# Kernel tuning notes

Measured on AMD Instinct MI355X. Metric: run time of the kernel, lower is better.

## Reference

```python
import jax, jax.numpy as jnp
import numpy as np

B, N, D = 8, 2048, 3
HIDDEN = (64, 128, 256)
LATENT = 128


def _layernorm(x, scale, bias, eps=1e-6):
    mu = jnp.mean(x, axis=-1, keepdims=True)
    var = jnp.mean((x - mu) ** 2, axis=-1, keepdims=True)
    return (x - mu) / jnp.sqrt(var + eps) * scale + bias


def setup_inputs() -> dict:
    key = jax.random.key(0)
    ks = jax.random.split(key, 8)
    inp = {
        "x": jax.random.normal(ks[0], (B, N, D), dtype=jnp.float32),
        "mask": jnp.ones((B, N), dtype=jnp.float32),
    }
    in_d = D
    for i, d in enumerate(HIDDEN):
        inp[f"W{i}"] = (jax.random.normal(ks[1 + i], (in_d, d), dtype=jnp.float32)
                        / np.float32(np.sqrt(in_d)))
        inp[f"b{i}"] = jnp.zeros((d,), dtype=jnp.float32)
        inp[f"g{i}"] = jnp.ones((d,), dtype=jnp.float32)
        inp[f"be{i}"] = jnp.zeros((d,), dtype=jnp.float32)
        in_d = d
    inp["Wz"] = (jax.random.normal(ks[5], (in_d, LATENT), dtype=jnp.float32)
                 / np.float32(np.sqrt(in_d)))
    inp["bz"] = jnp.zeros((LATENT,), dtype=jnp.float32)
    return inp


def reference(x, mask, W0, b0, g0, be0, W1, b1, g1, be1, W2, b2, g2, be2, Wz, bz):
    m = mask[..., None]                                   # (B, N, 1)
    count = jnp.sum(m, axis=1)                            # (B, 1)
    centroid = jnp.sum(x * m, axis=1, keepdims=True) / jnp.maximum(count, 1.0)[:, None, :]
    xc = x - centroid                                     # (B, N, D)

    # Pairwise squared distances; attention depends only on coordinates,
    # so it is identical for every layer -> compute once.
    diff = xc[:, :, None, :] - xc[:, None, :, :]          # (B, N, N, D)
    dist = jnp.sum(diff * diff, axis=-1)                  # (B, N, N)
    attn = jax.nn.softmax(-dist, axis=-1)                 # (B, N, N)

    h = xc
    for W, b, g, be in ((W0, b0, g0, be0), (W1, b1, g1, be1), (W2, b2, g2, be2)):
        h_agg = jnp.einsum('bij,bjd->bid', attn, h)       # weighted aggregation
        h = h_agg @ W + b
        h = _layernorm(h, g, be)
        h = jax.nn.swish(h)

    # Invariant readout: masked mean pool then Dense(latent)
    global_feat = jnp.sum(h * m, axis=1) / jnp.maximum(count, 1.0)
    z = global_feat @ Wz + bz                             # (B, latent)
    return z
```

## Files before the change

### kernel.cpp

```cpp
#include <hip/hip_runtime.h>
#include <hip/hip_bf16.h>

#define BATCH 8
#define NPTS 2048
#define LATENT 128

typedef __attribute__((ext_vector_type(8))) short short8;
typedef __attribute__((ext_vector_type(4))) float f32x4;

__device__ __forceinline__ ushort f2bf(float f) {
  unsigned int b = __float_as_uint(f);
  b += 0x7FFF + ((b >> 16) & 1);
  return (ushort)(b >> 16);
}
__device__ __forceinline__ float bf2f(ushort u) {
  return __uint_as_float(((unsigned int)u) << 16);
}
__device__ __forceinline__ unsigned int pkbf(float a, float b) {
  __hip_bfloat162 h = __float22bfloat162_rn(make_float2(a, b));
  return *(unsigned int*)&h;
}

#define L2E 1.4426950408889634f
#define SC2 1.6986436f

__device__ __forceinline__ void wtrans_tile(const float* __restrict__ W,
    ushort* __restrict__ WT, int K, int N, int n0, int k0, int tid) {
  __shared__ ushort s[64][72];
  for (int i = tid; i < 64 * 64; i += 256) {
    const int kl = i >> 6, nl = i & 63;
    s[kl][nl] = f2bf(W[(size_t)(k0 + kl) * N + n0 + nl]);
  }
  __syncthreads();
  for (int i = tid; i < 64 * 64; i += 256) {
    const int nl = i >> 6, kl = i & 63;
    WT[(size_t)(n0 + nl) * K + k0 + kl] = s[kl][nl];
  }
}

__global__ __launch_bounds__(256) void setup_kernel(const float* __restrict__ x,
    const float* __restrict__ mask, float4* __restrict__ pnt,
    const float* __restrict__ W1, ushort* __restrict__ WT1,
    const float* __restrict__ W2, ushort* __restrict__ WT2,
    const float* __restrict__ Wz, ushort* __restrict__ WzT) {
  const int bid = blockIdx.x;
  const int tid = threadIdx.x;
  if (bid >= 8) {
    if (bid < 10) wtrans_tile(W1, WT1, 64, 128, (bid - 8) * 64, 0, tid);
    else if (bid < 18) {
      const int idx = bid - 10;
      wtrans_tile(W2, WT2, 128, 256, (idx & 3) * 64, (idx >> 2) * 64, tid);
    } else {
      const int idx = bid - 18;
      wtrans_tile(Wz, WzT, 256, 128, (idx & 1) * 64, (idx >> 1) * 64, tid);
    }
    return;
  }
  const int b = bid;
  const float* xb = x + (size_t)b * NPTS * 3;
  const float* mb = mask + (size_t)b * NPTS;
  float s0 = 0.f, s1 = 0.f, s2 = 0.f, c = 0.f;
  for (int n = tid; n < NPTS; n += 256) {
    float m = mb[n];
    s0 += xb[n * 3 + 0] * m;
    s1 += xb[n * 3 + 1] * m;
    s2 += xb[n * 3 + 2] * m;
    c += m;
  }
  __shared__ float red[4][256];
  red[0][tid] = s0; red[1][tid] = s1; red[2][tid] = s2; red[3][tid] = c;
  __syncthreads();
  for (int off = 128; off > 0; off >>= 1) {
    if (tid < off) {
      red[0][tid] += red[0][tid + off];
      red[1][tid] += red[1][tid + off];
      red[2][tid] += red[2][tid + off];
      red[3][tid] += red[3][tid + off];
    }
    __syncthreads();
  }
  const float cnt = fmaxf(red[3][0], 1.0f);
  const float c0 = red[0][0] / cnt, c1 = red[1][0] / cnt, c2 = red[2][0] / cnt;
  float4* pb = pnt + (size_t)b * NPTS;
  for (int n = tid; n < NPTS; n += 256) {
    const float a0 = xb[n * 3 + 0] - c0;
    const float a1 = xb[n * 3 + 1] - c1;
    const float a2 = xb[n * 3 + 2] - c2;
    pb[n] = make_float4(a0 * SC2, a1 * SC2, a2 * SC2,
                        -(a0 * a0 + a1 * a1 + a2 * a2) * L2E);
  }
}

__global__ __launch_bounds__(512) void layer0_kernel(
    const float4* __restrict__ pnt, const float* __restrict__ W,
    const float* __restrict__ bias, const float* __restrict__ g,
    const float* __restrict__ be, ushort* __restrict__ hout) {
  const int b = blockIdx.y;
  const int i0 = blockIdx.x * 64;
  const int tid = threadIdx.x;
  const int il = tid & 63, part = tid >> 6;
  const float4* pb = pnt + (size_t)b * NPTS;
  const float4 pi = pb[i0 + il];
  float a0 = 0.f, a1 = 0.f, a2 = 0.f, dn = 0.f;
#pragma unroll 8
  for (int j = part * 256; j < part * 256 + 256; j++) {
    const float4 pj = pb[j];
    float arg = pi.w + pj.w;
    arg = fmaf(pi.x, pj.x, arg);
    arg = fmaf(pi.y, pj.y, arg);
    arg = fmaf(pi.z, pj.z, arg);
    const float w = __builtin_amdgcn_exp2f(arg);
    a0 = fmaf(w, pj.x, a0);
    a1 = fmaf(w, pj.y, a1);
    a2 = fmaf(w, pj.z, a2);
    dn += w;
  }
  __shared__ float4 sred[8][64];
  __shared__ float srow[64 * 3];
  __shared__ ushort lt[64][64];
  sred[part][il] = make_float4(a0, a1, a2, dn);
  __syncthreads();
  if (tid < 64) {
    float A0 = 0.f, A1 = 0.f, A2 = 0.f, DN = 0.f;
#pragma unroll
    for (int p = 0; p < 8; p++) {
      const float4 r = sred[p][tid];
      A0 += r.x; A1 += r.y; A2 += r.z; DN += r.w;
    }
    const float inv = 1.0f / (DN * SC2);
    srow[tid * 3 + 0] = A0 * inv;
    srow[tid * 3 + 1] = A1 * inv;
    srow[tid * 3 + 2] = A2 * inv;
  }
  __syncthreads();
  const int wv = tid >> 6, lane = tid & 63;
  const float w0c = W[lane], w1c = W[64 + lane], w2c = W[128 + lane];
  const float gv = g[lane], bev = be[lane], bv = bias[lane];
#pragma unroll
  for (int r = 0; r < 8; r++) {
    const int row = wv * 8 + r;
    float o = bv;
    o = fmaf(srow[row * 3 + 0], w0c, o);
    o = fmaf(srow[row * 3 + 1], w1c, o);
    o = fmaf(srow[row * 3 + 2], w2c, o);
    float m1 = o, m2 = o * o;
#pragma unroll
    for (int off = 32; off > 0; off >>= 1) {
      m1 += __shfl_xor(m1, off, 64);
      m2 += __shfl_xor(m2, off, 64);
    }
    const float mu = m1 / 64.f;
    const float rstd = rsqrtf(m2 / 64.f - mu * mu + 1e-6f);
    const float v = (o - mu) * rstd * gv + bev;
    const float act = v / (1.0f + __expf(-v));
    lt[row][lane] = f2bf(act);
  }
  __syncthreads();
  if (tid < 64) {
    ushort tmp[64];
#pragma unroll
    for (int r = 0; r < 64; r++) tmp[r] = lt[r][tid];
    ushort* dst = hout + ((size_t)b * 64 + tid) * NPTS + i0;
#pragma unroll
    for (int c = 0; c < 8; c++)
      *(uint4*)(dst + c * 8) = *(uint4*)&tmp[c * 8];
  }
}

template <int DIN, int DOUT, bool POOL, int MINW>
__global__ __launch_bounds__(256, MINW) void fused_layer(
    const float4* __restrict__ pnt, const ushort* __restrict__ hT,
    const ushort* __restrict__ WT, const float* __restrict__ bias,
    const float* __restrict__ g, const float* __restrict__ be,
    ushort* __restrict__ hout, const float* __restrict__ mask,
    float* __restrict__ partial) {
  constexpr int NT = DIN / 16;
  constexpr int QJ = NPTS / 4;
  constexpr int KS = QJ / 32;
  constexpr int NCOL = DOUT / 32;
  constexpr int PS = DIN + 8;
  constexpr int PN = DIN + 4;
  constexpr int SPNT_B = NPTS * 16;
  constexpr int SNUM_B = 32 * PN * 4;
  constexpr int OFF_SROW = SNUM_B;
  constexpr int OFF_SDEN = OFF_SROW + 32 * PS * 2;
  constexpr int OFF_SINV = OFF_SDEN + 128;
  constexpr int OFF_SSTAT = OFF_SINV + 128;
  constexpr int EPI_B = OFF_SSTAT + 512;
  constexpr int SMEM_B = SPNT_B > EPI_B ? SPNT_B : EPI_B;
  __shared__ __align__(16) char smem[SMEM_B];
  float4* sp = (float4*)smem;

  const int b = blockIdx.y;
  const int i0 = blockIdx.x * 32;
  const int tid = threadIdx.x;
  const int wv = tid >> 6, lane = tid & 63;
  const int m = lane & 15, q = lane >> 4;
  const float4* pb = pnt + (size_t)b * NPTS;
  const ushort* hb = hT + (size_t)b * DIN * NPTS;

#pragma unroll
  for (int i = 0; i < NPTS / 256; i++) {
    const int j = i * 256 + tid;
    const int phys = (j & ~31) | (((j & 7) << 2) | ((j >> 3) & 3));
    sp[phys] = pb[j];
  }
  const float4 pi0 = pb[i0 + m];
  const float4 pi1 = pb[i0 + 16 + m];
  __syncthreads();

  f32x4 acc0[NT], acc1[NT];
#pragma unroll
  for (int nt = 0; nt < NT; nt++)
#pragma unroll
    for (int e = 0; e < 4; e++) { acc0[nt][e] = 0.f; acc1[nt][e] = 0.f; }
  float dacc0 = 0.f, dacc1 = 0.f;

  const int jq = wv * QJ;

  for (int k = 0; k < KS; k++) {
    const int j0 = jq + k * 32;
    short8 bq[NT];
#pragma unroll
    for (int nt = 0; nt < NT; nt++)
      bq[nt] = *(const short8*)(hb + (size_t)(nt * 16 + m) * NPTS + j0 + q * 8);
    float w0a[8], w1a[8];
#pragma unroll
    for (int jj = 0; jj < 8; jj++) {
      const float4 pj = sp[j0 + ((jj << 2) | q)];
      float a0 = pi0.w + pj.w;
      a0 = fmaf(pi0.x, pj.x, a0);
      a0 = fmaf(pi0.y, pj.y, a0);
      a0 = fmaf(pi0.z, pj.z, a0);
      float a1 = pi1.w + pj.w;
      a1 = fmaf(pi1.x, pj.x, a1);
      a1 = fmaf(pi1.y, pj.y, a1);
      a1 = fmaf(pi1.z, pj.z, a1);
      w0a[jj] = __builtin_amdgcn_exp2f(a0);
      w1a[jj] = __builtin_amdgcn_exp2f(a1);
      dacc0 += w0a[jj]; dacc1 += w1a[jj];
    }
    unsigned int au0[4], au1[4];
#pragma unroll
    for (int p = 0; p < 4; p++) {
      au0[p] = pkbf(w0a[2 * p], w0a[2 * p + 1]);
      au1[p] = pkbf(w1a[2 * p], w1a[2 * p + 1]);
    }
    const short8 af0 = *(short8*)au0;
    const short8 af1 = *(short8*)au1;
#pragma unroll
    for (int nt = 0; nt < NT; nt++) {
      acc0[nt] = __builtin_amdgcn_mfma_f32_16x16x32_bf16(af0, bq[nt], acc0[nt], 0, 0, 0);
      acc1[nt] = __builtin_amdgcn_mfma_f32_16x16x32_bf16(af1, bq[nt], acc1[nt], 0, 0, 0);
    }
  }
  __syncthreads();

  float* snum = (float*)smem;
  ushort* srow = (ushort*)(smem + OFF_SROW);
  float* sden = (float*)(smem + OFF_SDEN);
  float* sinv = (float*)(smem + OFF_SINV);
  float* sstat = (float*)(smem + OFF_SSTAT);

  dacc0 += __shfl_xor(dacc0, 16, 64);
  dacc0 += __shfl_xor(dacc0, 32, 64);
  dacc1 += __shfl_xor(dacc1, 16, 64);
  dacc1 += __shfl_xor(dacc1, 32, 64);
  for (int p = 0; p < 4; p++) {
    if (wv == p) {
      if (p == 0) {
#pragma unroll
        for (int nt = 0; nt < NT; nt++)
#pragma unroll
          for (int r = 0; r < 4; r++) {
            snum[(q * 4 + r) * PN + nt * 16 + m] = acc0[nt][r];
            snum[(16 + q * 4 + r) * PN + nt * 16 + m] = acc1[nt][r];
          }
        if (q == 0) { sden[m] = dacc0; sden[16 + m] = dacc1; }
      } else {
#pragma unroll
        for (int nt = 0; nt < NT; nt++)
#pragma unroll
          for (int r = 0; r < 4; r++) {
            snum[(q * 4 + r) * PN + nt * 16 + m] += acc0[nt][r];
            snum[(16 + q * 4 + r) * PN + nt * 16 + m] += acc1[nt][r];
          }
        if (q == 0) { sden[m] += dacc0; sden[16 + m] += dacc1; }
      }
    }
    __syncthreads();
  }
  if (tid < 32) sinv[tid] = 1.0f / sden[tid];
  __syncthreads();
  for (int idx = tid; idx < 32 * (DIN / 2); idx += 256) {
    const int r = idx / (DIN / 2), c2 = idx % (DIN / 2);
    const float v0 = snum[r * PN + 2 * c2] * sinv[r];
    const float v1 = snum[r * PN + 2 * c2 + 1] * sinv[r];
    *(unsigned int*)&srow[r * PS + 2 * c2] = pkbf(v0, v1);
  }
  __syncthreads();

  const int rg2 = wv >> 1, ch = wv & 1;
  short8 afrag[DIN / 32];
#pragma unroll
  for (int kt = 0; kt < DIN / 32; kt++)
    afrag[kt] = *(const short8*)&srow[(rg2 * 16 + m) * PS + kt * 32 + q * 8];
  f32x4 oacc[NCOL];
#pragma unroll
  for (int c = 0; c < NCOL; c++)
#pragma unroll
    for (int e = 0; e < 4; e++) oacc[c][e] = 0.f;
#pragma unroll
  for (int c = 0; c < NCOL; c++) {
    const int n0 = (ch * NCOL + c) * 16;
#pragma unroll
    for (int kt = 0; kt < DIN / 32; kt++) {
      const short8 bfrag = *(const short8*)(WT + (size_t)(n0 + m) * DIN + kt * 32 + q * 8);
      oacc[c] = __builtin_amdgcn_mfma_f32_16x16x32_bf16(afrag[kt], bfrag, oacc[c], 0, 0, 0);
    }
  }

  float bcol[NCOL];
#pragma unroll
  for (int c = 0; c < NCOL; c++) bcol[c] = bias[(ch * NCOL + c) * 16 + m];
#pragma unroll
  for (int r = 0; r < 4; r++) {
    float m1 = 0.f, m2 = 0.f;
#pragma unroll
    for (int c = 0; c < NCOL; c++) {
      const float v = oacc[c][r] + bcol[c];
      m1 += v; m2 += v * v;
    }
#pragma unroll
    for (int off = 8; off > 0; off >>= 1) {
      m1 += __shfl_xor(m1, off, 64);
      m2 += __shfl_xor(m2, off, 64);
    }
    if (m == 0) {
      const int row = rg2 * 16 + q * 4 + r;
      sstat[(row * 2 + ch) * 2 + 0] = m1;
      sstat[(row * 2 + ch) * 2 + 1] = m2;
    }
  }
  __syncthreads();

  ushort* lt = (ushort*)smem;
  float* spl = (float*)smem;
  float pacc[NCOL];
  if (POOL) {
#pragma unroll
    for (int c = 0; c < NCOL; c++) pacc[c] = 0.f;
  }
#pragma unroll
  for (int r = 0; r < 4; r++) {
    const int row = rg2 * 16 + q * 4 + r;
    const float m1 = sstat[(row * 2 + 0) * 2 + 0] + sstat[(row * 2 + 1) * 2 + 0];
    const float m2 = sstat[(row * 2 + 0) * 2 + 1] + sstat[(row * 2 + 1) * 2 + 1];
    const float mu = m1 / DOUT;
    const float rstd = rsqrtf(m2 / DOUT - mu * mu + 1e-6f);
    float mval = 0.f;
    if (POOL) mval = mask[(size_t)b * NPTS + i0 + row];
#pragma unroll
    for (int c = 0; c < NCOL; c++) {
      const int dco = (ch * NCOL + c) * 16 + m;
      const float v = (oacc[c][r] + bcol[c] - mu) * rstd * g[dco] + be[dco];
      const float act = v / (1.0f + __expf(-v));
      if (POOL) pacc[c] = fmaf(act, mval, pacc[c]);
      else lt[row * DOUT + dco] = f2bf(act);
    }
  }
  if (POOL) {
#pragma unroll
    for (int c = 0; c < NCOL; c++) {
      float v = pacc[c];
      v += __shfl_xor(v, 16, 64);
      v += __shfl_xor(v, 32, 64);
      if (q == 0) spl[rg2 * DOUT + (ch * NCOL + c) * 16 + m] = v;
    }
    __syncthreads();
    if (tid < DOUT)
      partial[((size_t)b * (NPTS / 32) + blockIdx.x) * DOUT + tid] =
          spl[tid] + spl[DOUT + tid];
  } else {
    __syncthreads();
    if (tid < DOUT) {
      ushort tmp[32];
#pragma unroll
      for (int r = 0; r < 32; r++) tmp[r] = lt[r * DOUT + tid];
      ushort* dst = hout + ((size_t)b * DOUT + tid) * NPTS + i0;
#pragma unroll
      for (int c = 0; c < 4; c++)
        *(uint4*)(dst + c * 8) = *(uint4*)&tmp[c * 8];
    }
  }
}

__global__ __launch_bounds__(256) void readout_kernel(
    const float* __restrict__ partial, const float* __restrict__ mask,
    const ushort* __restrict__ WzT, const float* __restrict__ bz,
    float* __restrict__ out) {
  const int b = blockIdx.x;
  const int tid = threadIdx.x;
  const float* pb = partial + (size_t)b * (NPTS / 32) * 256;
  float s0 = 0.f, s1 = 0.f, s2 = 0.f, s3 = 0.f;
#pragma unroll 4
  for (int p = 0; p < NPTS / 32; p += 4) {
    s0 += pb[(size_t)(p + 0) * 256 + tid];
    s1 += pb[(size_t)(p + 1) * 256 + tid];
    s2 += pb[(size_t)(p + 2) * 256 + tid];
    s3 += pb[(size_t)(p + 3) * 256 + tid];
  }
  const float s = (s0 + s1) + (s2 + s3);
  const float* mb = mask + (size_t)b * NPTS;
  float c = 0.f;
  for (int n = tid; n < NPTS; n += 256) c += mb[n];
  __shared__ float red[256];
  red[tid] = c;
  __syncthreads();
  for (int off = 128; off > 0; off >>= 1) {
    if (tid < off) red[tid] += red[tid + off];
    __syncthreads();
  }
  const float cnt = fmaxf(red[0], 1.0f);
  __shared__ float gf[256];
  gf[tid] = s / cnt;
  __syncthreads();
  const int col = tid & 127, part = tid >> 7;
  float z = 0.f;
  const ushort* wr = WzT + (size_t)col * 256 + part * 128;
  const float* gp = gf + part * 128;
#pragma unroll 4
  for (int d = 0; d < 128; d += 8) {
    const short8 w8 = *(const short8*)(wr + d);
#pragma unroll
    for (int e = 0; e < 8; e++)
      z = fmaf(gp[d + e], bf2f((ushort)w8[e]), z);
  }
  __shared__ float zred[256];
  zred[tid] = z;
  __syncthreads();
  if (tid < LATENT)
    out[(size_t)b * LATENT + tid] = bz[tid] + zred[tid] + zred[128 + tid];
}

extern "C" void kernel_launch(void* const* d_in, const int* in_sizes, int n_in,
                              void* d_out, int out_size, void* d_ws, size_t ws_size,
                              hipStream_t stream) {
  const float* x    = (const float*)d_in[0];
  const float* mask = (const float*)d_in[1];
  const float* W0   = (const float*)d_in[2];
  const float* b0   = (const float*)d_in[3];
  const float* g0   = (const float*)d_in[4];
  const float* be0  = (const float*)d_in[5];
  const float* W1   = (const float*)d_in[6];
  const float* b1   = (const float*)d_in[7];
  const float* g1   = (const float*)d_in[8];
  const float* be1  = (const float*)d_in[9];
  const float* W2   = (const float*)d_in[10];
  const float* b2   = (const float*)d_in[11];
  const float* g2   = (const float*)d_in[12];
  const float* be2  = (const float*)d_in[13];
  const float* Wz   = (const float*)d_in[14];
  const float* bz   = (const float*)d_in[15];
  float* out = (float*)d_out;

  char* ws = (char*)d_ws;
  float4* pnt     = (float4*)(ws);
  ushort* h1T     = (ushort*)(ws + 262144);
  ushort* h2T     = (ushort*)(ws + 2359296);
  float*  partial = (float*)(ws + 6553600);
  ushort* WT1     = (ushort*)(ws + 7077888);
  ushort* WT2     = (ushort*)(ws + 7094272);
  ushort* WzT     = (ushort*)(ws + 7159808);

  setup_kernel<<<dim3(26), dim3(256), 0, stream>>>(
      x, mask, pnt, W1, WT1, W2, WT2, Wz, WzT);

  layer0_kernel<<<dim3(NPTS / 64, BATCH), dim3(512), 0, stream>>>(
      pnt, W0, b0, g0, be0, h1T);

  fused_layer<64, 128, false, 4><<<dim3(NPTS / 32, BATCH), dim3(256), 0, stream>>>(
      pnt, h1T, WT1, b1, g1, be1, h2T, nullptr, nullptr);

  fused_layer<128, 256, true, 3><<<dim3(NPTS / 32, BATCH), dim3(256), 0, stream>>>(
      pnt, h2T, WT2, b2, g2, be2, nullptr, mask, partial);

  readout_kernel<<<dim3(BATCH), dim3(256), 0, stream>>>(partial, mask, WzT, bz, out);
}
```

Baseline: 187.5 us.

## Use 512-thread blocks in fused layers, splitting key range across eight waves

Doubles the fused layer block size to 8 waves, so each wave covers an eighth of the key points instead of a quarter. Two groups of waves reduce partial numerators and denominators into separate shared-memory slots, which are then summed. The output projection is split four ways across columns, with layernorm statistics gathered from four partials. This is meant to add latency hiding per block and shorten each wave's serial key loop. The cost is more shared memory, a larger launch bound and higher register pressure, which may reduce occupancy. The key loop is also now fully unrolled.

```diff
diff --git a/kernel.cpp b/kernel.cpp
--- a/kernel.cpp
+++ b/kernel.cpp
@@ -167,26 +167,26 @@
   }
 }
 
-template <int DIN, int DOUT, bool POOL, int MINW>
-__global__ __launch_bounds__(256, MINW) void fused_layer(
+template <int DIN, int DOUT, bool POOL>
+__global__ __launch_bounds__(512, 4) void fused_layer(
     const float4* __restrict__ pnt, const ushort* __restrict__ hT,
     const ushort* __restrict__ WT, const float* __restrict__ bias,
     const float* __restrict__ g, const float* __restrict__ be,
     ushort* __restrict__ hout, const float* __restrict__ mask,
     float* __restrict__ partial) {
   constexpr int NT = DIN / 16;
-  constexpr int QJ = NPTS / 4;
+  constexpr int QJ = NPTS / 8;
   constexpr int KS = QJ / 32;
-  constexpr int NCOL = DOUT / 32;
+  constexpr int NCOL = DOUT / 64;
   constexpr int PS = DIN + 8;
   constexpr int PN = DIN + 4;
   constexpr int SPNT_B = NPTS * 16;
-  constexpr int SNUM_B = 32 * PN * 4;
-  constexpr int OFF_SROW = SNUM_B;
+  constexpr int SLOT_B = 32 * PN * 4;
+  constexpr int OFF_SROW = 2 * SLOT_B;
   constexpr int OFF_SDEN = OFF_SROW + 32 * PS * 2;
-  constexpr int OFF_SINV = OFF_SDEN + 128;
+  constexpr int OFF_SINV = OFF_SDEN + 256;
   constexpr int OFF_SSTAT = OFF_SINV + 128;
-  constexpr int EPI_B = OFF_SSTAT + 512;
+  constexpr int EPI_B = OFF_SSTAT + 1024;
   constexpr int SMEM_B = SPNT_B > EPI_B ? SPNT_B : EPI_B;
   __shared__ __align__(16) char smem[SMEM_B];
   float4* sp = (float4*)smem;
@@ -200,8 +200,8 @@
   const ushort* hb = hT + (size_t)b * DIN * NPTS;
 
 #pragma unroll
-  for (int i = 0; i < NPTS / 256; i++) {
-    const int j = i * 256 + tid;
+  for (int i = 0; i < NPTS / 512; i++) {
+    const int j = i * 512 + tid;
     const int phys = (j & ~31) | (((j & 7) << 2) | ((j >> 3) & 3));
     sp[phys] = pb[j];
   }
@@ -217,17 +217,18 @@
   float dacc0 = 0.f, dacc1 = 0.f;
 
   const int jq = wv * QJ;
-
+  const ushort* hrow = hb + (size_t)m * NPTS + jq + q * 8;
+
+#pragma unroll
   for (int k = 0; k < KS; k++) {
-    const int j0 = jq + k * 32;
     short8 bq[NT];
 #pragma unroll
     for (int nt = 0; nt < NT; nt++)
-      bq[nt] = *(const short8*)(hb + (size_t)(nt * 16 + m) * NPTS + j0 + q * 8);
+      bq[nt] = *(const short8*)(hrow + (size_t)nt * 16 * NPTS + k * 32);
     float w0a[8], w1a[8];
 #pragma unroll
     for (int jj = 0; jj < 8; jj++) {
-      const float4 pj = sp[j0 + ((jj << 2) | q)];
+      const float4 pj = sp[jq + k * 32 + ((jj << 2) | q)];
       float a0 = pi0.w + pj.w;
       a0 = fmaf(pi0.x, pj.x, a0);
       a0 = fmaf(pi0.y, pj.y, a0);
@@ -256,7 +257,8 @@
   }
   __syncthreads();
 
-  float* snum = (float*)smem;
+  float* snum0 = (float*)smem;
+  float* snum1 = (float*)(smem + SLOT_B);
   ushort* srow = (ushort*)(smem + OFF_SROW);
   float* sden = (float*)(smem + OFF_SDEN);
   float* sinv = (float*)(smem + OFF_SINV);
@@ -266,41 +268,47 @@
   dacc0 += __shfl_xor(dacc0, 32, 64);
   dacc1 += __shfl_xor(dacc1, 16, 64);
   dacc1 += __shfl_xor(dacc1, 32, 64);
-  for (int p = 0; p < 4; p++) {
-    if (wv == p) {
-      if (p == 0) {
-#pragma unroll
-        for (int nt = 0; nt < NT; nt++)
-#pragma unroll
-          for (int r = 0; r < 4; r++) {
-            snum[(q * 4 + r) * PN + nt * 16 + m] = acc0[nt][r];
-            snum[(16 + q * 4 + r) * PN + nt * 16 + m] = acc1[nt][r];
-          }
-        if (q == 0) { sden[m] = dacc0; sden[16 + m] = dacc1; }
-      } else {
-#pragma unroll
-        for (int nt = 0; nt < NT; nt++)
-#pragma unroll
-          for (int r = 0; r < 4; r++) {
-            snum[(q * 4 + r) * PN + nt * 16 + m] += acc0[nt][r];
-            snum[(16 + q * 4 + r) * PN + nt * 16 + m] += acc1[nt][r];
-          }
-        if (q == 0) { sden[m] += dacc0; sden[16 + m] += dacc1; }
+  {
+    const int grp = wv >> 2;
+    float* sn = grp ? snum1 : snum0;
+    float* sd = sden + grp * 32;
+    const int ph = wv & 3;
+    for (int p = 0; p < 4; p++) {
+      if (ph == p) {
+        if (p == 0) {
+#pragma unroll
+          for (int nt = 0; nt < NT; nt++)
+#pragma unroll
+            for (int r = 0; r < 4; r++) {
+              sn[(q * 4 + r) * PN + nt * 16 + m] = acc0[nt][r];
+              sn[(16 + q * 4 + r) * PN + nt * 16 + m] = acc1[nt][r];
+            }
+          if (q == 0) { sd[m] = dacc0; sd[16 + m] = dacc1; }
+        } else {
+#pragma unroll
+          for (int nt = 0; nt < NT; nt++)
+#pragma unroll
+            for (int r = 0; r < 4; r++) {
+              sn[(q * 4 + r) * PN + nt * 16 + m] += acc0[nt][r];
+              sn[(16 + q * 4 + r) * PN + nt * 16 + m] += acc1[nt][r];
+            }
+          if (q == 0) { sd[m] += dacc0; sd[16 + m] += dacc1; }
+        }
       }
-    }
-    __syncthreads();
-  }
-  if (tid < 32) sinv[tid] = 1.0f / sden[tid];
-  __syncthreads();
-  for (int idx = tid; idx < 32 * (DIN / 2); idx += 256) {
+      __syncthreads();
+    }
+  }
+  if (tid < 32) sinv[tid] = 1.0f / (sden[tid] + sden[32 + tid]);
+  __syncthreads();
+  for (int idx = tid; idx < 32 * (DIN / 2); idx += 512) {
     const int r = idx / (DIN / 2), c2 = idx % (DIN / 2);
-    const float v0 = snum[r * PN + 2 * c2] * sinv[r];
-    const float v1 = snum[r * PN + 2 * c2 + 1] * sinv[r];
+    const float v0 = (snum0[r * PN + 2 * c2] + snum1[r * PN + 2 * c2]) * sinv[r];
+    const float v1 = (snum0[r * PN + 2 * c2 + 1] + snum1[r * PN + 2 * c2 + 1]) * sinv[r];
     *(unsigned int*)&srow[r * PS + 2 * c2] = pkbf(v0, v1);
   }
   __syncthreads();
 
-  const int rg2 = wv >> 1, ch = wv & 1;
+  const int rg2 = wv >> 2, ch = wv & 3;
   short8 afrag[DIN / 32];
 #pragma unroll
   for (int kt = 0; kt < DIN / 32; kt++)
@@ -338,8 +346,8 @@
     }
     if (m == 0) {
       const int row = rg2 * 16 + q * 4 + r;
-      sstat[(row * 2 + ch) * 2 + 0] = m1;
-      sstat[(row * 2 + ch) * 2 + 1] = m2;
+      sstat[(row * 4 + ch) * 2 + 0] = m1;
+      sstat[(row * 4 + ch) * 2 + 1] = m2;
     }
   }
   __syncthreads();
@@ -354,8 +362,10 @@
 #pragma unroll
   for (int r = 0; r < 4; r++) {
     const int row = rg2 * 16 + q * 4 + r;
-    const float m1 = sstat[(row * 2 + 0) * 2 + 0] + sstat[(row * 2 + 1) * 2 + 0];
-    const float m2 = sstat[(row * 2 + 0) * 2 + 1] + sstat[(row * 2 + 1) * 2 + 1];
+    const float m1 = (sstat[(row * 4 + 0) * 2 + 0] + sstat[(row * 4 + 1) * 2 + 0]) +
+                     (sstat[(row * 4 + 2) * 2 + 0] + sstat[(row * 4 + 3) * 2 + 0]);
+    const float m2 = (sstat[(row * 4 + 0) * 2 + 1] + sstat[(row * 4 + 1) * 2 + 1]) +
+                     (sstat[(row * 4 + 2) * 2 + 1] + sstat[(row * 4 + 3) * 2 + 1]);
     const float mu = m1 / DOUT;
     const float rstd = rsqrtf(m2 / DOUT - mu * mu + 1e-6f);
     float mval = 0.f;
@@ -479,10 +489,10 @@
   layer0_kernel<<<dim3(NPTS / 64, BATCH), dim3(512), 0, stream>>>(
       pnt, W0, b0, g0, be0, h1T);
 
-  fused_layer<64, 128, false, 4><<<dim3(NPTS / 32, BATCH), dim3(256), 0, stream>>>(
+  fused_layer<64, 128, false><<<dim3(NPTS / 32, BATCH), dim3(512), 0, stream>>>(
       pnt, h1T, WT1, b1, g1, be1, h2T, nullptr, nullptr);
 
-  fused_layer<128, 256, true, 3><<<dim3(NPTS / 32, BATCH), dim3(256), 0, stream>>>(
+  fused_layer<128, 256, true><<<dim3(NPTS / 32, BATCH), dim3(512), 0, stream>>>(
       pnt, h2T, WT2, b2, g2, be2, nullptr, mask, partial);
 
   readout_kernel<<<dim3(BATCH), dim3(256), 0, stream>>>(partial, mask, WzT, bz, out);
```

Result: slower. 220.7 us (+17.7%).

## Halve query rows per block in fused attention layers to 16

Applied to the files above, without the earlier changes.

Each fused_layer block now handles 16 query points instead of 32. This halves the MFMA accumulators and doubles the grid, and all four waves share one row group in the dense epilogue, with LayerNorm stats reduced across four column chunks. The goal is to lower register pressure so occupancy can rise (launch bounds now 4 for both layers). The cost is that every h^T tile and the point-cloud copy in shared memory are loaded twice as often per output row. The partial-sum buffer and the readout loop grow to match, and the workspace offsets move.

```diff
diff --git a/kernel.cpp b/kernel.cpp
--- a/kernel.cpp
+++ b/kernel.cpp
@@ -167,8 +167,8 @@
   }
 }
 
-template <int DIN, int DOUT, bool POOL, int MINW>
-__global__ __launch_bounds__(256, MINW) void fused_layer(
+template <int DIN, int DOUT, bool POOL>
+__global__ __launch_bounds__(256, 4) void fused_layer(
     const float4* __restrict__ pnt, const ushort* __restrict__ hT,
     const ushort* __restrict__ WT, const float* __restrict__ bias,
     const float* __restrict__ g, const float* __restrict__ be,
@@ -177,22 +177,22 @@
   constexpr int NT = DIN / 16;
   constexpr int QJ = NPTS / 4;
   constexpr int KS = QJ / 32;
-  constexpr int NCOL = DOUT / 32;
+  constexpr int NCOL = DOUT / 64;
   constexpr int PS = DIN + 8;
   constexpr int PN = DIN + 4;
   constexpr int SPNT_B = NPTS * 16;
-  constexpr int SNUM_B = 32 * PN * 4;
+  constexpr int SNUM_B = 16 * PN * 4;
   constexpr int OFF_SROW = SNUM_B;
-  constexpr int OFF_SDEN = OFF_SROW + 32 * PS * 2;
-  constexpr int OFF_SINV = OFF_SDEN + 128;
-  constexpr int OFF_SSTAT = OFF_SINV + 128;
+  constexpr int OFF_SDEN = OFF_SROW + 16 * PS * 2;
+  constexpr int OFF_SINV = OFF_SDEN + 64;
+  constexpr int OFF_SSTAT = OFF_SINV + 64;
   constexpr int EPI_B = OFF_SSTAT + 512;
   constexpr int SMEM_B = SPNT_B > EPI_B ? SPNT_B : EPI_B;
   __shared__ __align__(16) char smem[SMEM_B];
   float4* sp = (float4*)smem;
 
   const int b = blockIdx.y;
-  const int i0 = blockIdx.x * 32;
+  const int i0 = blockIdx.x * 16;
   const int tid = threadIdx.x;
   const int wv = tid >> 6, lane = tid & 63;
   const int m = lane & 15, q = lane >> 4;
@@ -205,16 +205,15 @@
     const int phys = (j & ~31) | (((j & 7) << 2) | ((j >> 3) & 3));
     sp[phys] = pb[j];
   }
-  const float4 pi0 = pb[i0 + m];
-  const float4 pi1 = pb[i0 + 16 + m];
-  __syncthreads();
-
-  f32x4 acc0[NT], acc1[NT];
+  const float4 pi = pb[i0 + m];
+  __syncthreads();
+
+  f32x4 acc[NT];
 #pragma unroll
   for (int nt = 0; nt < NT; nt++)
 #pragma unroll
-    for (int e = 0; e < 4; e++) { acc0[nt][e] = 0.f; acc1[nt][e] = 0.f; }
-  float dacc0 = 0.f, dacc1 = 0.f;
+    for (int e = 0; e < 4; e++) acc[nt][e] = 0.f;
+  float dacc = 0.f;
 
   const int jq = wv * QJ;
 
@@ -224,35 +223,24 @@
 #pragma unroll
     for (int nt = 0; nt < NT; nt++)
       bq[nt] = *(const short8*)(hb + (size_t)(nt * 16 + m) * NPTS + j0 + q * 8);
-    float w0a[8], w1a[8];
+    float wa[8];
 #pragma unroll
     for (int jj = 0; jj < 8; jj++) {
       const float4 pj = sp[j0 + ((jj << 2) | q)];
-      float a0 = pi0.w + pj.w;
-      a0 = fmaf(pi0.x, pj.x, a0);
-      a0 = fmaf(pi0.y, pj.y, a0);
-      a0 = fmaf(pi0.z, pj.z, a0);
-      float a1 = pi1.w + pj.w;
-      a1 = fmaf(pi1.x, pj.x, a1);
-      a1 = fmaf(pi1.y, pj.y, a1);
-      a1 = fmaf(pi1.z, pj.z, a1);
-      w0a[jj] = __builtin_amdgcn_exp2f(a0);
-      w1a[jj] = __builtin_amdgcn_exp2f(a1);
-      dacc0 += w0a[jj]; dacc1 += w1a[jj];
-    }
-    unsigned int au0[4], au1[4];
-#pragma unroll
-    for (int p = 0; p < 4; p++) {
-      au0[p] = pkbf(w0a[2 * p], w0a[2 * p + 1]);
-      au1[p] = pkbf(w1a[2 * p], w1a[2 * p + 1]);
-    }
-    const short8 af0 = *(short8*)au0;
-    const short8 af1 = *(short8*)au1;
-#pragma unroll
-    for (int nt = 0; nt < NT; nt++) {
-      acc0[nt] = __builtin_amdgcn_mfma_f32_16x16x32_bf16(af0, bq[nt], acc0[nt], 0, 0, 0);
-      acc1[nt] = __builtin_amdgcn_mfma_f32_16x16x32_bf16(af1, bq[nt], acc1[nt], 0, 0, 0);
-    }
+      float a0 = pi.w + pj.w;
+      a0 = fmaf(pi.x, pj.x, a0);
+      a0 = fmaf(pi.y, pj.y, a0);
+      a0 = fmaf(pi.z, pj.z, a0);
+      wa[jj] = __builtin_amdgcn_exp2f(a0);
+      dacc += wa[jj];
+    }
+    unsigned int au[4];
+#pragma unroll
+    for (int p = 0; p < 4; p++) au[p] = pkbf(wa[2 * p], wa[2 * p + 1]);
+    const short8 af = *(short8*)au;
+#pragma unroll
+    for (int nt = 0; nt < NT; nt++)
+      acc[nt] = __builtin_amdgcn_mfma_f32_16x16x32_bf16(af, bq[nt], acc[nt], 0, 0, 0);
   }
   __syncthreads();
 
@@ -262,37 +250,31 @@
   float* sinv = (float*)(smem + OFF_SINV);
   float* sstat = (float*)(smem + OFF_SSTAT);
 
-  dacc0 += __shfl_xor(dacc0, 16, 64);
-  dacc0 += __shfl_xor(dacc0, 32, 64);
-  dacc1 += __shfl_xor(dacc1, 16, 64);
-  dacc1 += __shfl_xor(dacc1, 32, 64);
+  dacc += __shfl_xor(dacc, 16, 64);
+  dacc += __shfl_xor(dacc, 32, 64);
   for (int p = 0; p < 4; p++) {
     if (wv == p) {
       if (p == 0) {
 #pragma unroll
         for (int nt = 0; nt < NT; nt++)
 #pragma unroll
-          for (int r = 0; r < 4; r++) {
-            snum[(q * 4 + r) * PN + nt * 16 + m] = acc0[nt][r];
-            snum[(16 + q * 4 + r) * PN + nt * 16 + m] = acc1[nt][r];
-          }
-        if (q == 0) { sden[m] = dacc0; sden[16 + m] = dacc1; }
+          for (int r = 0; r < 4; r++)
+            snum[(q * 4 + r) * PN + nt * 16 + m] = acc[nt][r];
+        if (q == 0) sden[m] = dacc;
       } else {
 #pragma unroll
         for (int nt = 0; nt < NT; nt++)
 #pragma unroll
-          for (int r = 0; r < 4; r++) {
-            snum[(q * 4 + r) * PN + nt * 16 + m] += acc0[nt][r];
-            snum[(16 + q * 4 + r) * PN + nt * 16 + m] += acc1[nt][r];
-          }
-        if (q == 0) { sden[m] += dacc0; sden[16 + m] += dacc1; }
+          for (int r = 0; r < 4; r++)
+            snum[(q * 4 + r) * PN + nt * 16 + m] += acc[nt][r];
+        if (q == 0) sden[m] += dacc;
       }
     }
     __syncthreads();
   }
-  if (tid < 32) sinv[tid] = 1.0f / sden[tid];
-  __syncthreads();
-  for (int idx = tid; idx < 32 * (DIN / 2); idx += 256) {
+  if (tid < 16) sinv[tid] = 1.0f / sden[tid];
+  __syncthreads();
+  for (int idx = tid; idx < 16 * (DIN / 2); idx += 256) {
     const int r = idx / (DIN / 2), c2 = idx % (DIN / 2);
     const float v0 = snum[r * PN + 2 * c2] * sinv[r];
     const float v1 = snum[r * PN + 2 * c2 + 1] * sinv[r];
@@ -300,11 +282,11 @@
   }
   __syncthreads();
 
-  const int rg2 = wv >> 1, ch = wv & 1;
+  const int ch = wv;
   short8 afrag[DIN / 32];
 #pragma unroll
   for (int kt = 0; kt < DIN / 32; kt++)
-    afrag[kt] = *(const short8*)&srow[(rg2 * 16 + m) * PS + kt * 32 + q * 8];
+    afrag[kt] = *(const short8*)&srow[m * PS + kt * 32 + q * 8];
   f32x4 oacc[NCOL];
 #pragma unroll
   for (int c = 0; c < NCOL; c++)
@@ -337,9 +319,9 @@
       m2 += __shfl_xor(m2, off, 64);
     }
     if (m == 0) {
-      const int row = rg2 * 16 + q * 4 + r;
-      sstat[(row * 2 + ch) * 2 + 0] = m1;
-      sstat[(row * 2 + ch) * 2 + 1] = m2;
+      const int row = q * 4 + r;
+      sstat[(row * 4 + ch) * 2 + 0] = m1;
+      sstat[(row * 4 + ch) * 2 + 1] = m2;
     }
   }
   __syncthreads();
@@ -353,9 +335,11 @@
   }
 #pragma unroll
   for (int r = 0; r < 4; r++) {
-    const int row = rg2 * 16 + q * 4 + r;
-    const float m1 = sstat[(row * 2 + 0) * 2 + 0] + sstat[(row * 2 + 1) * 2 + 0];
-    const float m2 = sstat[(row * 2 + 0) * 2 + 1] + sstat[(row * 2 + 1) * 2 + 1];
+    const int row = q * 4 + r;
+    const float m1 = (sstat[(row * 4 + 0) * 2 + 0] + sstat[(row * 4 + 1) * 2 + 0]) +
+                     (sstat[(row * 4 + 2) * 2 + 0] + sstat[(row * 4 + 3) * 2 + 0]);
+    const float m2 = (sstat[(row * 4 + 0) * 2 + 1] + sstat[(row * 4 + 1) * 2 + 1]) +
+                     (sstat[(row * 4 + 2) * 2 + 1] + sstat[(row * 4 + 3) * 2 + 1]);
     const float mu = m1 / DOUT;
     const float rstd = rsqrtf(m2 / DOUT - mu * mu + 1e-6f);
     float mval = 0.f;
@@ -375,22 +359,20 @@
       float v = pacc[c];
       v += __shfl_xor(v, 16, 64);
       v += __shfl_xor(v, 32, 64);
-      if (q == 0) spl[rg2 * DOUT + (ch * NCOL + c) * 16 + m] = v;
+      if (q == 0) spl[(ch * NCOL + c) * 16 + m] = v;
     }
     __syncthreads();
     if (tid < DOUT)
-      partial[((size_t)b * (NPTS / 32) + blockIdx.x) * DOUT + tid] =
-          spl[tid] + spl[DOUT + tid];
+      partial[((size_t)b * (NPTS / 16) + blockIdx.x) * DOUT + tid] = spl[tid];
   } else {
     __syncthreads();
     if (tid < DOUT) {
-      ushort tmp[32];
-#pragma unroll
-      for (int r = 0; r < 32; r++) tmp[r] = lt[r * DOUT + tid];
+      ushort tmp[16];
+#pragma unroll
+      for (int r = 0; r < 16; r++) tmp[r] = lt[r * DOUT + tid];
       ushort* dst = hout + ((size_t)b * DOUT + tid) * NPTS + i0;
-#pragma unroll
-      for (int c = 0; c < 4; c++)
-        *(uint4*)(dst + c * 8) = *(uint4*)&tmp[c * 8];
+      *(uint4*)dst = *(uint4*)&tmp[0];
+      *(uint4*)(dst + 8) = *(uint4*)&tmp[8];
     }
   }
 }
@@ -401,10 +383,10 @@
     float* __restrict__ out) {
   const int b = blockIdx.x;
   const int tid = threadIdx.x;
-  const float* pb = partial + (size_t)b * (NPTS / 32) * 256;
+  const float* pb = partial + (size_t)b * (NPTS / 16) * 256;
   float s0 = 0.f, s1 = 0.f, s2 = 0.f, s3 = 0.f;
 #pragma unroll 4
-  for (int p = 0; p < NPTS / 32; p += 4) {
+  for (int p = 0; p < NPTS / 16; p += 4) {
     s0 += pb[(size_t)(p + 0) * 256 + tid];
     s1 += pb[(size_t)(p + 1) * 256 + tid];
     s2 += pb[(size_t)(p + 2) * 256 + tid];
@@ -469,9 +451,9 @@
   ushort* h1T     = (ushort*)(ws + 262144);
   ushort* h2T     = (ushort*)(ws + 2359296);
   float*  partial = (float*)(ws + 6553600);
-  ushort* WT1     = (ushort*)(ws + 7077888);
-  ushort* WT2     = (ushort*)(ws + 7094272);
-  ushort* WzT     = (ushort*)(ws + 7159808);
+  ushort* WT1     = (ushort*)(ws + 7602176);
+  ushort* WT2     = (ushort*)(ws + 7618560);
+  ushort* WzT     = (ushort*)(ws + 7684096);
 
   setup_kernel<<<dim3(26), dim3(256), 0, stream>>>(
       x, mask, pnt, W1, WT1, W2, WT2, Wz, WzT);
@@ -479,10 +461,10 @@
   layer0_kernel<<<dim3(NPTS / 64, BATCH), dim3(512), 0, stream>>>(
       pnt, W0, b0, g0, be0, h1T);
 
-  fused_layer<64, 128, false, 4><<<dim3(NPTS / 32, BATCH), dim3(256), 0, stream>>>(
+  fused_layer<64, 128, false><<<dim3(NPTS / 16, BATCH), dim3(256), 0, stream>>>(
       pnt, h1T, WT1, b1, g1, be1, h2T, nullptr, nullptr);
 
-  fused_layer<128, 256, true, 3><<<dim3(NPTS / 32, BATCH), dim3(256), 0, stream>>>(
+  fused_layer<128, 256, true><<<dim3(NPTS / 16, BATCH), dim3(256), 0, stream>>>(
       pnt, h2T, WT2, b2, g2, be2, nullptr, mask, partial);
 
   readout_kernel<<<dim3(BATCH), dim3(256), 0, stream>>>(partial, mask, WzT, bz, out);
```

Result: slower. 224.9 us (+19.9%).
